# Kernel tuning notes

Hardware: AMD Instinct MI355X
Metric: run time of the kernel (lower is better)

## Reference

```python
import jax, jax.numpy as jnp
import numpy as np

NUM_CLUSTERS = 32


def setup_inputs() -> dict:
    key = jax.random.key(0)
    k1, k2 = jax.random.split(key)
    B, N, D = 16, 16384, 128
    x = jax.random.normal(k1, (B, N, D), dtype=jnp.float32)
    cluster_ids = jax.random.randint(k2, (B, N), 0, NUM_CLUSTERS, dtype=jnp.int32)
    return {"x": x, "cluster_ids": cluster_ids}


def reference(x, cluster_ids):
    # x: [B, N, D]; cluster_ids: [B, N] int labels in [0, C)
    C = NUM_CLUSTERS
    # One-hot cluster membership: [B, N, C]
    onehot = (cluster_ids[..., None] == jnp.arange(C, dtype=cluster_ids.dtype)).astype(x.dtype)
    counts = onehot.sum(axis=1)                       # [B, C]
    sums = jnp.einsum('bnc,bnd->bcd', onehot, x)      # segment sums [B, C, D]
    # Per-cluster mean; empty clusters -> zero rows (contribute 0 to off-diag Gram)
    means = sums / jnp.maximum(counts, 1.0)[..., None]
    # Pairwise |dot products| between cluster means: [B, C, C]
    gram = jnp.abs(jnp.einsum('bcd,bed->bce', means, means))
    # Strict upper-triangular sum (torch.triu(..., diagonal=1))
    triu_mask = jnp.triu(jnp.ones((C, C), dtype=x.dtype), k=1)
    triu_sum = jnp.sum(gram * triu_mask, axis=(1, 2))  # [B]
    # Number of valid (non-empty) clusters per batch
    valid = jnp.sum(counts > 0, axis=1).astype(x.dtype)
    denom = jnp.where(valid > 1, valid * (valid - 1.0) * 0.5, 1.0)
    return jnp.mean(triu_sum / denom)
```

## Files before the change

kernel.cpp:

```cpp
#include <hip/hip_runtime.h>
#include <hip/hip_bf16.h>

#define BB 16
#define NN 16384
#define DD 128
#define CC 32
#define CHUNKS 16
#define NBLK (BB * CHUNKS)
#define ROWS_PER_BLOCK (NN / CHUNKS)

#define P_SUMS 0
#define P_CNTS ((size_t)NBLK * CC * DD)
#define LOSSP  (P_CNTS + (size_t)NBLK * CC)
#define GCTR   (LOSSP + BB)
#define WS_A_FLOATS (GCTR + 1)

__global__ __launch_bounds__(512) void seg_sum_kernel(
    const float* __restrict__ x, const int* __restrict__ ids,
    float* __restrict__ outsums, float* __restrict__ outcnts,
    int* __restrict__ gctr) {
  __shared__ float slab[8][CC * 64];
  __shared__ float lcnt[CC];
  __shared__ int   lcid[ROWS_PER_BLOCK];

  const int tid  = threadIdx.x;
  const int b    = blockIdx.y;
  const int row0 = blockIdx.x * ROWS_PER_BLOCK;
  const int lane = tid & 63;
  const int w    = tid >> 6;
  const int rr   = w >> 1;
  const int h    = w & 1;
  const int slot = b * CHUNKS + blockIdx.x;
  const int* __restrict__ idrow = ids + (size_t)b * NN;

  if (tid < CC) lcnt[tid] = 0.f;
  lcid[tid]       = idrow[row0 + tid];
  lcid[tid + 512] = idrow[row0 + tid + 512];
  {
    const float4 z4 = make_float4(0.f, 0.f, 0.f, 0.f);
#pragma unroll
    for (int i = 0; i < 8; ++i)
      *reinterpret_cast<float4*>(&slab[w][(i * 64 + lane) * 4]) = z4;
  }
  __syncthreads();
  atomicAdd(&lcnt[lcid[tid]], 1.f);
  atomicAdd(&lcnt[lcid[tid + 512]], 1.f);

  const float* __restrict__ p0 =
      x + ((size_t)b * NN + row0 + rr * 256) * DD + h * 64 + lane;
  const int kb0 = rr * 256;
  float* const sl = &slab[w][0];

  float vA[8], vB[8];
  int cA[8], cB[8];

#define LOADG(V, C, g)                                                     \
  {                                                                        \
    _Pragma("unroll") for (int k = 0; k < 8; ++k) {                        \
      V[k] = __builtin_nontemporal_load(&p0[((g) * 8 + k) * DD]);          \
      C[k] = lcid[kb0 + (g) * 8 + k];                                      \
    }                                                                      \
  }
#define RMWG(V, C)                                                         \
  {                                                                        \
    _Pragma("unroll") for (int k = 0; k < 8; ++k) {                        \
      float* p = &sl[C[k] * 64 + lane];                                    \
      *p = *p + V[k];                                                      \
    }                                                                      \
  }

  LOADG(vA, cA, 0)
#pragma unroll
  for (int i = 0; i < 15; ++i) {
    LOADG(vB, cB, 2 * i + 1)
    RMWG(vA, cA)
    LOADG(vA, cA, 2 * i + 2)
    RMWG(vB, cB)
  }
  LOADG(vB, cB, 31)
  RMWG(vA, cA)
  RMWG(vB, cB)
#undef LOADG
#undef RMWG
  __syncthreads();

  float* __restrict__ ps = outsums + (size_t)slot * CC * DD;
#pragma unroll
  for (int it = 0; it < 8; ++it) {
    const int idx = it * 512 + tid;
    const int c  = idx >> 7;
    const int r  = idx & 127;
    const int h2 = r >> 6;
    const int j  = r & 63;
    const int o  = c * 64 + j;
    ps[idx] = slab[h2][o] + slab[2 + h2][o] + slab[4 + h2][o] + slab[6 + h2][o];
  }
  if (tid < CC) outcnts[slot * CC + tid] = lcnt[tid];
  if (slot == 0 && tid == 0)
    __hip_atomic_store(gctr, 0, __ATOMIC_RELAXED, __HIP_MEMORY_SCOPE_AGENT);
}

#define MSTR 132
__global__ __launch_bounds__(512) void finish_fused_kernel(
    const float* __restrict__ psums, const float* __restrict__ pcnts,
    float* __restrict__ lossp, int* __restrict__ gctr,
    float* __restrict__ out) {
  __shared__ float mean[CC * MSTR];
  __shared__ float cnt[CC];
  __shared__ float red[512];

  const int b = blockIdx.x;
  const int tid = threadIdx.x;

  if (tid < CC) {
    float cs = 0.f;
#pragma unroll
    for (int c = 0; c < CHUNKS; ++c) cs += pcnts[(b * CHUNKS + c) * CC + tid];
    cnt[tid] = cs;
  }

  float4 a0 = make_float4(0.f, 0.f, 0.f, 0.f), a1 = a0;
  const size_t base = (size_t)b * CHUNKS * CC * DD + (size_t)tid * 8;
#pragma unroll 4
  for (int c = 0; c < CHUNKS; ++c) {
    const float4* p = reinterpret_cast<const float4*>(&psums[base + (size_t)c * CC * DD]);
    float4 q0 = p[0], q1 = p[1];
    a0.x += q0.x; a0.y += q0.y; a0.z += q0.z; a0.w += q0.w;
    a1.x += q1.x; a1.y += q1.y; a1.z += q1.z; a1.w += q1.w;
  }
  __syncthreads();

  {
    const int c = tid >> 4;
    const int d0 = (tid & 15) * 8;
    const float inv = 1.f / fmaxf(cnt[c], 1.f);
    float* mrow = &mean[c * MSTR + d0];
    mrow[0] = a0.x * inv; mrow[1] = a0.y * inv; mrow[2] = a0.z * inv; mrow[3] = a0.w * inv;
    mrow[4] = a1.x * inv; mrow[5] = a1.y * inv; mrow[6] = a1.z * inv; mrow[7] = a1.w * inv;
  }
  __syncthreads();

  float acc = 0.f;
  if (tid < (CC * (CC - 1)) / 2) {
    int c = 0, rem = tid;
    while (rem >= (CC - 1 - c)) { rem -= (CC - 1 - c); ++c; }
    int e = c + 1 + rem;
    const float4* mc = reinterpret_cast<const float4*>(&mean[c * MSTR]);
    const float4* me = reinterpret_cast<const float4*>(&mean[e * MSTR]);
    float dot = 0.f;
#pragma unroll 8
    for (int j = 0; j < DD / 4; ++j) {
      float4 u = mc[j], v = me[j];
      dot += u.x * v.x + u.y * v.y + u.z * v.z + u.w * v.w;
    }
    acc = fabsf(dot);
  }

  red[tid] = acc;
  __syncthreads();
  for (int s = 256; s > 0; s >>= 1) {
    if (tid < s) red[tid] += red[tid + s];
    __syncthreads();
  }

  if (tid == 0) {
    float valid = 0.f;
    for (int c = 0; c < CC; ++c) valid += (cnt[c] > 0.f) ? 1.f : 0.f;
    float denom = (valid > 1.f) ? valid * (valid - 1.f) * 0.5f : 1.f;
    float v = red[0] / denom * (1.0f / BB);
    __hip_atomic_store(&lossp[b], v, __ATOMIC_RELAXED, __HIP_MEMORY_SCOPE_AGENT);
    __threadfence();
    int old = __hip_atomic_fetch_add(gctr, 1, __ATOMIC_ACQ_REL,
                                     __HIP_MEMORY_SCOPE_AGENT);
    if (old == BB - 1) {
      __threadfence();
      float s = 0.f;
#pragma unroll
      for (int i = 0; i < BB; ++i)
        s += __hip_atomic_load(&lossp[i], __ATOMIC_RELAXED,
                               __HIP_MEMORY_SCOPE_AGENT);
      out[0] = s;
    }
  }
}

#define RPB_B 512
#define ROWS_PER_WAVE_B 128
__global__ __launch_bounds__(256) void seg_sum_rmw_b(
    const float* __restrict__ x, const int* __restrict__ ids,
    float* __restrict__ gsums, float* __restrict__ gcounts) {
  __shared__ float lsum[4][CC * DD];
  __shared__ float lcnt[CC];
  __shared__ int   lcid[RPB_B];

  const int tid  = threadIdx.x;
  const int b    = blockIdx.y;
  const int row0 = blockIdx.x * RPB_B;
  const int lane = tid & 63;
  const int w    = tid >> 6;
  const int* __restrict__ idrow = ids + (size_t)b * NN;

  if (tid < CC) lcnt[tid] = 0.f;
  lcid[tid]       = idrow[row0 + tid];
  lcid[tid + 256] = idrow[row0 + tid + 256];
  {
    const float4 z4 = make_float4(0.f, 0.f, 0.f, 0.f);
#pragma unroll
    for (int i = 0; i < 16; ++i)
      *reinterpret_cast<float4*>(&lsum[w][(i * 64 + lane) * 4]) = z4;
  }
  __syncthreads();
  atomicAdd(&lcnt[lcid[tid]], 1.f);
  atomicAdd(&lcnt[lcid[tid + 256]], 1.f);

  const float2* __restrict__ x2 =
      reinterpret_cast<const float2*>(x + (size_t)b * NN * DD);
  const int wbase = w * ROWS_PER_WAVE_B;
  float* const slab = &lsum[w][0];

  for (int g = 0; g < ROWS_PER_WAVE_B / 8; ++g) {
    float2 v[8]; int cid[8];
#pragma unroll
    for (int k = 0; k < 8; ++k) {
      const int rl = wbase + g * 8 + k;
      v[k]   = x2[(size_t)(row0 + rl) * 64 + lane];
      cid[k] = lcid[rl];
    }
#pragma unroll
    for (int k = 0; k < 8; ++k) {
      float2* p = reinterpret_cast<float2*>(&slab[cid[k] * DD + 2 * lane]);
      float2 old = *p;
      *p = make_float2(old.x + v[k].x, old.y + v[k].y);
    }
  }
  __syncthreads();

  float* __restrict__ gs = gsums + (size_t)b * CC * DD;
  for (int i = tid; i < CC * DD; i += 256) {
    float s = lsum[0][i] + lsum[1][i] + lsum[2][i] + lsum[3][i];
    atomicAdd(&gs[i], s);
  }
  if (tid < CC) atomicAdd(&gcounts[b * CC + tid], lcnt[tid]);
}

__global__ __launch_bounds__(512) void finish_kernel_b(
    const float* __restrict__ gsums, const float* __restrict__ gcounts,
    float* __restrict__ out) {
  __shared__ float mean[CC * MSTR];
  __shared__ float cnt[CC];
  __shared__ float red[512];

  const int b = blockIdx.x;
  const int tid = threadIdx.x;

  if (tid < CC) cnt[tid] = gcounts[b * CC + tid];
  __syncthreads();
  for (int i = tid; i < CC * DD; i += 512) {
    int c = i >> 7;
    int d = i & 127;
    mean[c * MSTR + d] = gsums[(size_t)b * CC * DD + i] / fmaxf(cnt[c], 1.f);
  }
  __syncthreads();

  float acc = 0.f;
  if (tid < (CC * (CC - 1)) / 2) {
    int c = 0, rem = tid;
    while (rem >= (CC - 1 - c)) { rem -= (CC - 1 - c); ++c; }
    int e = c + 1 + rem;
    const float4* mc = reinterpret_cast<const float4*>(&mean[c * MSTR]);
    const float4* me = reinterpret_cast<const float4*>(&mean[e * MSTR]);
    float dot = 0.f;
#pragma unroll 8
    for (int jj = 0; jj < DD / 4; ++jj) {
      float4 u = mc[jj], v = me[jj];
      dot += u.x * v.x + u.y * v.y + u.z * v.z + u.w * v.w;
    }
    acc = fabsf(dot);
  }
  red[tid] = acc;
  __syncthreads();
  for (int s = 256; s > 0; s >>= 1) {
    if (tid < s) red[tid] += red[tid + s];
    __syncthreads();
  }
  if (tid == 0) {
    float valid = 0.f;
    for (int c = 0; c < CC; ++c) valid += (cnt[c] > 0.f) ? 1.f : 0.f;
    float denom = (valid > 1.f) ? valid * (valid - 1.f) * 0.5f : 1.f;
    atomicAdd(out, red[0] / denom * (1.0f / BB));
  }
}

extern "C" void kernel_launch(void* const* d_in, const int* in_sizes, int n_in,
                              void* d_out, int out_size, void* d_ws, size_t ws_size,
                              hipStream_t stream) {
  const float* x   = (const float*)d_in[0];
  const int*   ids = (const int*)d_in[1];
  float* out = (float*)d_out;
  float* ws  = (float*)d_ws;

  if (ws_size >= WS_A_FLOATS * sizeof(float)) {
    float* psums = ws + P_SUMS;
    float* pcnts = ws + P_CNTS;
    float* lossp = ws + LOSSP;
    int*   gctr  = (int*)(ws + GCTR);
    dim3 grid1(CHUNKS, BB);
    seg_sum_kernel<<<grid1, 512, 0, stream>>>(x, ids, psums, pcnts, gctr);
    finish_fused_kernel<<<BB, 512, 0, stream>>>(psums, pcnts, lossp, gctr, out);
  } else {
    float* gsums   = ws;
    float* gcounts = gsums + (size_t)BB * CC * DD;
    const size_t wsb = ((size_t)BB * CC * DD + (size_t)BB * CC) * sizeof(float);
    hipMemsetAsync(d_ws, 0, wsb, stream);
    hipMemsetAsync(d_out, 0, sizeof(float), stream);
    dim3 gridb(NN / RPB_B, BB);
    seg_sum_rmw_b<<<gridb, 256, 0, stream>>>(x, ids, gsums, gcounts);
    finish_kernel_b<<<BB, 512, 0, stream>>>(gsums, gcounts, out);
  }
}
```

Baseline: 38.07 us.

## Stream x rows into LDS with async global_load_lds four-stage pipeline

Replaces the register double-buffered nontemporal loads with direct global-to-LDS async loads (16-byte per lane) into a per-wave 4-slot staging ring, using explicit vmcnt waits to keep three groups in flight while the current group is accumulated into the shared slab. The goal is deeper memory-level parallelism and lower register pressure on the bandwidth-bound segment-sum pass. It adds 64 KB of LDS per block, which may cut occupancy, and relies on hand-written waitcnt sequencing that could be fragile.

```diff
diff --git a/kernel.cpp b/kernel.cpp
--- a/kernel.cpp
+++ b/kernel.cpp
@@ -15,11 +15,15 @@
 #define GCTR   (LOSSP + BB)
 #define WS_A_FLOATS (GCTR + 1)
 
+typedef __attribute__((address_space(1))) const unsigned int glb_u32;
+typedef __attribute__((address_space(3))) unsigned int lds_u32;
+
 __global__ __launch_bounds__(512) void seg_sum_kernel(
     const float* __restrict__ x, const int* __restrict__ ids,
     float* __restrict__ outsums, float* __restrict__ outcnts,
     int* __restrict__ gctr) {
   __shared__ float slab[8][CC * 64];
+  __shared__ float stage[8][4][512];
   __shared__ float lcnt[CC];
   __shared__ int   lcid[ROWS_PER_BLOCK];
 
@@ -45,43 +49,51 @@
   __syncthreads();
   atomicAdd(&lcnt[lcid[tid]], 1.f);
   atomicAdd(&lcnt[lcid[tid + 512]], 1.f);
-
-  const float* __restrict__ p0 =
-      x + ((size_t)b * NN + row0 + rr * 256) * DD + h * 64 + lane;
+  __syncthreads();
+
+  const float* gsrc = x + ((size_t)b * NN + row0 + rr * 256 + (lane >> 4)) * DD
+                        + h * 64 + (lane & 15) * 4;
+  float* const sl = &slab[w][0];
   const int kb0 = rr * 256;
-  float* const sl = &slab[w][0];
-
-  float vA[8], vB[8];
-  int cA[8], cB[8];
-
-#define LOADG(V, C, g)                                                     \
-  {                                                                        \
-    _Pragma("unroll") for (int k = 0; k < 8; ++k) {                        \
-      V[k] = __builtin_nontemporal_load(&p0[((g) * 8 + k) * DD]);          \
-      C[k] = lcid[kb0 + (g) * 8 + k];                                      \
-    }                                                                      \
-  }
-#define RMWG(V, C)                                                         \
-  {                                                                        \
-    _Pragma("unroll") for (int k = 0; k < 8; ++k) {                        \
-      float* p = &sl[C[k] * 64 + lane];                                    \
-      *p = *p + V[k];                                                      \
-    }                                                                      \
-  }
-
-  LOADG(vA, cA, 0)
-#pragma unroll
-  for (int i = 0; i < 15; ++i) {
-    LOADG(vB, cB, 2 * i + 1)
-    RMWG(vA, cA)
-    LOADG(vA, cA, 2 * i + 2)
-    RMWG(vB, cB)
-  }
-  LOADG(vB, cB, 31)
-  RMWG(vA, cA)
-  RMWG(vB, cB)
-#undef LOADG
-#undef RMWG
+
+#define ISSUE(g)                                                            \
+  {                                                                         \
+    asm volatile("s_waitcnt lgkmcnt(0)" ::: "memory");                      \
+    __builtin_amdgcn_global_load_lds(                                       \
+        (glb_u32*)(gsrc + ((g) * 8 + 0) * DD),                              \
+        (lds_u32*)&stage[w][(g) & 3][0], 16, 0, 0);                         \
+    __builtin_amdgcn_global_load_lds(                                       \
+        (glb_u32*)(gsrc + ((g) * 8 + 4) * DD),                              \
+        (lds_u32*)&stage[w][(g) & 3][256], 16, 0, 0);                       \
+  }
+#define CONSUME(g)                                                          \
+  {                                                                         \
+    _Pragma("unroll") for (int j = 0; j < 8; ++j) {                         \
+      const float v = stage[w][(g) & 3][j * 64 + lane];                     \
+      const int cid = lcid[kb0 + (g) * 8 + j];                              \
+      float* p = &sl[cid * 64 + lane];                                      \
+      *p = *p + v;                                                          \
+    }                                                                       \
+  }
+
+  ISSUE(0) ISSUE(1) ISSUE(2)
+  for (int g = 0; g < 29; ++g) {
+    ISSUE(g + 3)
+    asm volatile("s_waitcnt vmcnt(6)" ::: "memory");
+    __builtin_amdgcn_sched_barrier(0);
+    CONSUME(g)
+  }
+  asm volatile("s_waitcnt vmcnt(4)" ::: "memory");
+  __builtin_amdgcn_sched_barrier(0);
+  CONSUME(29)
+  asm volatile("s_waitcnt vmcnt(2)" ::: "memory");
+  __builtin_amdgcn_sched_barrier(0);
+  CONSUME(30)
+  asm volatile("s_waitcnt vmcnt(0)" ::: "memory");
+  __builtin_amdgcn_sched_barrier(0);
+  CONSUME(31)
+#undef ISSUE
+#undef CONSUME
   __syncthreads();
 
   float* __restrict__ ps = outsums + (size_t)slot * CC * DD;
```

Result: slower. 43.01 us (+13.0%).

## Use float4 row loads with per-wave full-width LDS slabs for segment sums

Applied to the files above, without the earlier changes.

The segment-sum kernel now has each wave read whole rows as float4 vectors, instead of pairs of waves splitting rows into 64-column halves with scalar nontemporal loads. Each wave gets a full 32x128 LDS accumulator, with columns stored in a strided order (m, m+32, m+64, m+96), and the final reduction sums all eight wave slabs. The goal is wider, more efficient global loads on this memory-bound pass. In exchange the kernel doubles LDS use per block, which limits occupancy, and drops the nontemporal hint. The permuted column order is only safe because the downstream Gram computation is invariant to a consistent permutation of D.

```diff
diff --git a/kernel.cpp b/kernel.cpp
--- a/kernel.cpp
+++ b/kernel.cpp
@@ -19,7 +19,7 @@
     const float* __restrict__ x, const int* __restrict__ ids,
     float* __restrict__ outsums, float* __restrict__ outcnts,
     int* __restrict__ gctr) {
-  __shared__ float slab[8][CC * 64];
+  __shared__ float slab[8][CC * DD];
   __shared__ float lcnt[CC];
   __shared__ int   lcid[ROWS_PER_BLOCK];
 
@@ -28,8 +28,8 @@
   const int row0 = blockIdx.x * ROWS_PER_BLOCK;
   const int lane = tid & 63;
   const int w    = tid >> 6;
-  const int rr   = w >> 1;
-  const int h    = w & 1;
+  const int pr   = lane >> 5;
+  const int m    = lane & 31;
   const int slot = b * CHUNKS + blockIdx.x;
   const int* __restrict__ idrow = ids + (size_t)b * NN;
 
@@ -39,45 +39,49 @@
   {
     const float4 z4 = make_float4(0.f, 0.f, 0.f, 0.f);
 #pragma unroll
-    for (int i = 0; i < 8; ++i)
+    for (int i = 0; i < 16; ++i)
       *reinterpret_cast<float4*>(&slab[w][(i * 64 + lane) * 4]) = z4;
   }
   __syncthreads();
   atomicAdd(&lcnt[lcid[tid]], 1.f);
   atomicAdd(&lcnt[lcid[tid + 512]], 1.f);
 
-  const float* __restrict__ p0 =
-      x + ((size_t)b * NN + row0 + rr * 256) * DD + h * 64 + lane;
-  const int kb0 = rr * 256;
+  const float4* __restrict__ x4 = reinterpret_cast<const float4*>(
+      x + ((size_t)b * NN + row0) * DD);
+  const int wbase = w * 128;
   float* const sl = &slab[w][0];
 
-  float vA[8], vB[8];
+  float4 vA[8], vB[8];
   int cA[8], cB[8];
 
 #define LOADG(V, C, g)                                                     \
   {                                                                        \
     _Pragma("unroll") for (int k = 0; k < 8; ++k) {                        \
-      V[k] = __builtin_nontemporal_load(&p0[((g) * 8 + k) * DD]);          \
-      C[k] = lcid[kb0 + (g) * 8 + k];                                      \
+      const int rl = wbase + (g) * 16 + k * 2 + pr;                        \
+      V[k] = x4[(size_t)rl * 32 + m];                                      \
+      C[k] = lcid[rl];                                                     \
     }                                                                      \
   }
 #define RMWG(V, C)                                                         \
   {                                                                        \
     _Pragma("unroll") for (int k = 0; k < 8; ++k) {                        \
-      float* p = &sl[C[k] * 64 + lane];                                    \
-      *p = *p + V[k];                                                      \
+      float* p = &sl[C[k] * DD + m];                                       \
+      p[0]  += V[k].x;                                                     \
+      p[32] += V[k].y;                                                     \
+      p[64] += V[k].z;                                                     \
+      p[96] += V[k].w;                                                     \
     }                                                                      \
   }
 
   LOADG(vA, cA, 0)
 #pragma unroll
-  for (int i = 0; i < 15; ++i) {
+  for (int i = 0; i < 3; ++i) {
     LOADG(vB, cB, 2 * i + 1)
     RMWG(vA, cA)
     LOADG(vA, cA, 2 * i + 2)
     RMWG(vB, cB)
   }
-  LOADG(vB, cB, 31)
+  LOADG(vB, cB, 7)
   RMWG(vA, cA)
   RMWG(vB, cB)
 #undef LOADG
@@ -88,12 +92,9 @@
 #pragma unroll
   for (int it = 0; it < 8; ++it) {
     const int idx = it * 512 + tid;
-    const int c  = idx >> 7;
-    const int r  = idx & 127;
-    const int h2 = r >> 6;
-    const int j  = r & 63;
-    const int o  = c * 64 + j;
-    ps[idx] = slab[h2][o] + slab[2 + h2][o] + slab[4 + h2][o] + slab[6 + h2][o];
+    float s = slab[0][idx] + slab[1][idx] + slab[2][idx] + slab[3][idx] +
+              slab[4][idx] + slab[5][idx] + slab[6][idx] + slab[7][idx];
+    ps[idx] = s;
   }
   if (tid < CC) outcnts[slot * CC + tid] = lcnt[tid];
   if (slot == 0 && tid == 0)
```

Result: faster. 36.49 us (-4.2%).

## Interleave row assignment across blocks and use float2 loads with split half-wave slabs

Applied to the files above, without the earlier changes.

Each block now processes rows strided by 64 across the batch instead of a contiguous chunk. Each wave loads float2 values from two rows at once into separate half-wave shared slabs, and groups are visited in a batch-rotated order. This aims to spread DRAM traffic across channels and halve the per-thread load count. The cost is a doubled shared-memory footprint, which may lower occupancy, and the plain loads replace nontemporal ones.

```diff
diff --git a/kernel.cpp b/kernel.cpp
--- a/kernel.cpp
+++ b/kernel.cpp
@@ -19,65 +19,78 @@
     const float* __restrict__ x, const int* __restrict__ ids,
     float* __restrict__ outsums, float* __restrict__ outcnts,
     int* __restrict__ gctr) {
-  __shared__ float slab[8][CC * 64];
+  __shared__ __align__(16) float slabs[4][2][2][CC * 64];
   __shared__ float lcnt[CC];
-  __shared__ int   lcid[ROWS_PER_BLOCK];
+  __shared__ int   lcid[4][256];
 
   const int tid  = threadIdx.x;
   const int b    = blockIdx.y;
-  const int row0 = blockIdx.x * ROWS_PER_BLOCK;
+  const int cx   = blockIdx.x;
   const int lane = tid & 63;
   const int w    = tid >> 6;
-  const int rr   = w >> 1;
+  const int q    = w >> 1;
   const int h    = w & 1;
-  const int slot = b * CHUNKS + blockIdx.x;
+  const int pr   = lane >> 5;
+  const int m    = lane & 31;
+  const int slot = b * CHUNKS + cx;
   const int* __restrict__ idrow = ids + (size_t)b * NN;
 
   if (tid < CC) lcnt[tid] = 0.f;
-  lcid[tid]       = idrow[row0 + tid];
-  lcid[tid + 512] = idrow[row0 + tid + 512];
-  {
+  {
+    const int e0 = tid, e1 = tid + 512;
+    lcid[e0 >> 8][e0 & 255] = idrow[cx * 4 + (e0 >> 8) + 64 * (e0 & 255)];
+    lcid[e1 >> 8][e1 & 255] = idrow[cx * 4 + (e1 >> 8) + 64 * (e1 & 255)];
+  }
+  {
+    float* sb = &slabs[0][0][0][0];
     const float4 z4 = make_float4(0.f, 0.f, 0.f, 0.f);
 #pragma unroll
-    for (int i = 0; i < 8; ++i)
-      *reinterpret_cast<float4*>(&slab[w][(i * 64 + lane) * 4]) = z4;
-  }
-  __syncthreads();
-  atomicAdd(&lcnt[lcid[tid]], 1.f);
-  atomicAdd(&lcnt[lcid[tid + 512]], 1.f);
-
-  const float* __restrict__ p0 =
-      x + ((size_t)b * NN + row0 + rr * 256) * DD + h * 64 + lane;
-  const int kb0 = rr * 256;
-  float* const sl = &slab[w][0];
-
-  float vA[8], vB[8];
+    for (int i = 0; i < 16; ++i)
+      *reinterpret_cast<float4*>(&sb[(i * 512 + tid) * 4]) = z4;
+  }
+  __syncthreads();
+  {
+    const int e0 = tid, e1 = tid + 512;
+    atomicAdd(&lcnt[lcid[e0 >> 8][e0 & 255]], 1.f);
+    atomicAdd(&lcnt[lcid[e1 >> 8][e1 & 255]], 1.f);
+  }
+
+  const int srow = cx * 4 + q;
+  const float2* __restrict__ x2 =
+      reinterpret_cast<const float2*>(x + (size_t)b * NN * DD);
+  float* const sl = &slabs[q][h][pr][0];
+  const int colo = h * 32 + m;
+
+  float2 vA[8], vB[8];
   int cA[8], cB[8];
 
 #define LOADG(V, C, g)                                                     \
   {                                                                        \
+    const int ge = ((g) + b) & 15;              \
     _Pragma("unroll") for (int k = 0; k < 8; ++k) {                        \
-      V[k] = __builtin_nontemporal_load(&p0[((g) * 8 + k) * DD]);          \
-      C[k] = lcid[kb0 + (g) * 8 + k];                                      \
+      const int t = 2 * (ge * 8 + k) + pr;                                 \
+      V[k] = x2[(size_t)(srow + 64 * t) * 64 + colo];                      \
+      C[k] = lcid[q][t];                                                   \
     }                                                                      \
   }
 #define RMWG(V, C)                                                         \
   {                                                                        \
     _Pragma("unroll") for (int k = 0; k < 8; ++k) {                        \
-      float* p = &sl[C[k] * 64 + lane];                                    \
-      *p = *p + V[k];                                                      \
+      float2* p = reinterpret_cast<float2*>(&sl[C[k] * 64 + 2 * m]);       \
+      float2 old = *p;                                                     \
+      *p = make_float2(old.x + V[k].x, old.y + V[k].y);                    \
     }                                                                      \
   }
 
   LOADG(vA, cA, 0)
 #pragma unroll
-  for (int i = 0; i < 15; ++i) {
+  for (int i = 0; i < 7; ++i) {
     LOADG(vB, cB, 2 * i + 1)
     RMWG(vA, cA)
     LOADG(vA, cA, 2 * i + 2)
     RMWG(vB, cB)
   }
-  LOADG(vB, cB, 31)
+  LOADG(vB, cB, 15)
   RMWG(vA, cA)
   RMWG(vB, cB)
 #undef LOADG
@@ -93,7 +106,11 @@
     const int h2 = r >> 6;
     const int j  = r & 63;
     const int o  = c * 64 + j;
-    ps[idx] = slab[h2][o] + slab[2 + h2][o] + slab[4 + h2][o] + slab[6 + h2][o];
+    float s = 0.f;
+#pragma unroll
+    for (int qq = 0; qq < 4; ++qq)
+      s += slabs[qq][h2][0][o] + slabs[qq][h2][1][o];
+    ps[idx] = s;
   }
   if (tid < CC) outcnts[slot * CC + tid] = lcnt[tid];
   if (slot == 0 && tid == 0)
```

After: 36.57 us. -4.0%, faster.
